# Optimization experiments

Hardware: AMD Instinct MI355X
Metric: run time of the kernel (lower is better)

Reference implementation:

```python
import jax, jax.numpy as jnp
import numpy as np

PS = 8  # patch_size
EPS = 1e-5


def _layernorm(t, w, b):
    m = jnp.mean(t, axis=-1, keepdims=True)
    v = jnp.mean((t - m) ** 2, axis=-1, keepdims=True)
    return (t - m) * jax.lax.rsqrt(v + EPS) * w + b


def _to3d(t):  # B(HW)C -> BCHW
    B, N, C = t.shape
    H = W = int(np.sqrt(N))
    return t.reshape(B, H, W, C).transpose(0, 3, 1, 2)


def _to2d(t):  # BCHW -> B(HW)C
    B, C, H, W = t.shape
    return t.reshape(B, C, H * W).swapaxes(-1, -2)


def _block(t, ps=PS):  # BCHW -> [B, M, ps*ps, C] (dilated-grid blocking, as in torch code)
    B, C, H, W = t.shape
    t = t.reshape(B, C, ps, H // ps, ps, W // ps)
    t = t.transpose(0, 3, 5, 2, 4, 1)
    return t.reshape(B, (H * W) // (ps * ps), ps * ps, C)


def _unblock(t):  # inverse of _block
    B, M, N, C = t.shape
    Hb = Wb = int(np.sqrt(M))
    ps = int(np.sqrt(N))
    t = t.reshape(B, Hb, Wb, ps, ps, C)
    t = t.transpose(0, 5, 3, 1, 4, 2)
    return t.reshape(B, C, Hb * ps, Wb * ps)


def setup_inputs() -> dict:
    key = jax.random.key(0)
    ks = jax.random.split(key, 8)
    B, N, D, H = 8, 4096, 256, 8
    s = 1.0 / np.sqrt(D)
    return {
        "x": jax.random.normal(ks[0], (B, N, D), jnp.float32),
        "ln1_w": jnp.ones((D,), jnp.float32),
        "ln1_b": jnp.zeros((D,), jnp.float32),
        "q": jax.random.normal(ks[1], (H, D, D), jnp.float32) * s,
        "k": jax.random.normal(ks[2], (D, D), jnp.float32) * s,
        "v": jax.random.normal(ks[3], (D, D), jnp.float32) * s,
        "o": jax.random.normal(ks[4], (H, D, D), jnp.float32) * s,
        "ln2_w": jnp.ones((D,), jnp.float32),
        "ln2_b": jnp.zeros((D,), jnp.float32),
        "w1": jax.random.normal(ks[5], (D, D), jnp.float32) * s,
        "b1": jnp.zeros((D,), jnp.float32),
        "w2": jax.random.normal(ks[6], (D, D), jnp.float32) * s,
        "b2": jnp.zeros((D,), jnp.float32),
    }


def reference(x, ln1_w, ln1_b, q, k, v, o, ln2_w, ln2_b, w1, b1, w2, b2):
    # blocked input: [B, M, P, D], M = HW/ps^2, P = ps^2
    a = _block(_to3d(_layernorm(x, ln1_w, ln1_b)))
    nh = q.shape[0]
    Q = jnp.einsum('bmnd,hdk->bhmnk', a, q)
    Q1, Q2 = Q[:, : nh // 2], Q[:, nh // 2 :]
    K = jnp.einsum('bmnd,dk->bmnk', a, k)
    V = jnp.einsum('bmnd,dv->bmnv', a, v)
    # axis 1: attend across blocks (m) at fixed within-block position (y=n)
    s1 = jax.nn.softmax(jnp.einsum('bhxyk,bzyk->bhyxz', Q1, K), axis=-1)
    O1 = jnp.einsum('bhyxz,bzyv->bhxyv', s1, V)
    # axis 2: attend within block (n) at fixed block (x=m)
    s2 = jax.nn.softmax(jnp.einsum('bhxyk,bxzk->bhxyz', Q2, K), axis=-1)
    O2 = jnp.einsum('bhxyz,bxzv->bhxyv', s2, V)
    O = jnp.concatenate([O1, O2], axis=1)  # [B, H, M, P, D]
    # faithful to torch: 'bhmnd,hdv->bmnd' sums over h and v
    Z = jnp.einsum('bhmnd,hdv->bmnd', O, o)
    x = x + _to2d(_unblock(Z))
    h = _layernorm(x, ln2_w, ln2_b)
    mlp = jax.nn.relu(h @ w1 + b1) @ w2 + b2
    return x + mlp
```

## Files before the change

### kernel.cpp

```cpp
#include <hip/hip_runtime.h>

#define Bc   8
#define Tc   4096
#define Dc   256
#define EPSc 1e-5f

typedef _Float16 half_t;
typedef __attribute__((ext_vector_type(4))) _Float16 half4_t;
typedef __attribute__((ext_vector_type(8))) _Float16 frag8;
typedef __attribute__((ext_vector_type(4))) float f32x4;

#define MFMA_F16(a, b, c) __builtin_amdgcn_mfma_f32_16x16x32_f16((a), (b), (c), 0, 0, 0)

__global__ __launch_bounds__(256) void osum_kernel(const float* __restrict__ o, float* __restrict__ os) {
  int h = blockIdx.x, d = threadIdx.x;
  const float* row = o + ((size_t)h * 256 + d) * 256;
  float s = 0.f;
  #pragma unroll 8
  for (int v = 0; v < 256; v += 4) {
    float4 r4 = *(const float4*)&row[v];
    s += r4.x + r4.y + r4.z + r4.w;
  }
  os[h * 256 + d] = s;
}

__global__ __launch_bounds__(256) void prepM_kernel(const float* __restrict__ q,
                                                    const float* __restrict__ k,
                                                    half_t* __restrict__ Mt) {
  __shared__ float shK[32 * 260];
  __shared__ float shQ[32 * 260];
  int tid = threadIdx.x;
  int h = blockIdx.x >> 6, et = (blockIdx.x >> 3) & 7, dt = blockIdx.x & 7;
  const float* kbase = k + (size_t)(et * 32) * 256;
  const float* qbase = q + ((size_t)h * 256 + dt * 32) * 256;
  #pragma unroll
  for (int r = 0; r < 8; r++) {
    int f = r * 256 + tid;
    int row = f >> 6, c4 = (f & 63) * 4;
    *(float4*)&shK[row * 260 + c4] = *(const float4*)&kbase[(size_t)row * 256 + c4];
    *(float4*)&shQ[row * 260 + c4] = *(const float4*)&qbase[(size_t)row * 256 + c4];
  }
  __syncthreads();
  int e = tid & 31, dg = tid >> 5;
  const float* kr = &shK[e * 260];
  const float* q0 = &shQ[(dg * 4 + 0) * 260];
  const float* q1 = &shQ[(dg * 4 + 1) * 260];
  const float* q2 = &shQ[(dg * 4 + 2) * 260];
  const float* q3 = &shQ[(dg * 4 + 3) * 260];
  float a0 = 0.f, a1 = 0.f, a2 = 0.f, a3 = 0.f;
  #pragma unroll 4
  for (int kk = 0; kk < 256; kk += 4) {
    float4 kv = *(const float4*)&kr[kk];
    float4 v0 = *(const float4*)&q0[kk];
    float4 v1 = *(const float4*)&q1[kk];
    float4 v2 = *(const float4*)&q2[kk];
    float4 v3 = *(const float4*)&q3[kk];
    a0 += v0.x * kv.x + v0.y * kv.y + v0.z * kv.z + v0.w * kv.w;
    a1 += v1.x * kv.x + v1.y * kv.y + v1.z * kv.z + v1.w * kv.w;
    a2 += v2.x * kv.x + v2.y * kv.y + v2.z * kv.z + v2.w * kv.w;
    a3 += v3.x * kv.x + v3.y * kv.y + v3.z * kv.z + v3.w * kv.w;
  }
  half4_t outv;
  outv[0] = (half_t)a0; outv[1] = (half_t)a1; outv[2] = (half_t)a2; outv[3] = (half_t)a3;
  *(half4_t*)&Mt[((size_t)h * 256 + et * 32 + e) * 256 + dt * 32 + dg * 4] = outv;
}

__global__ __launch_bounds__(256) void prepT_kernel(const float* __restrict__ v,
                                                    const float* __restrict__ w1,
                                                    const float* __restrict__ w2,
                                                    half_t* vt, half_t* w1t, half_t* w2t) {
  int which = blockIdx.x >> 8, n = blockIdx.x & 255, d = threadIdx.x;
  const float* src = which == 0 ? v : (which == 1 ? w1 : w2);
  half_t* dst = which == 0 ? vt : (which == 1 ? w1t : w2t);
  dst[(size_t)n * 256 + d] = (half_t)src[(size_t)d * 256 + n];
}

__global__ __launch_bounds__(256) void ln1_kernel(
    const float* __restrict__ x, const float* __restrict__ w,
    const float* __restrict__ bia, half_t* __restrict__ aH) {
  int row  = blockIdx.x * 4 + (threadIdx.x >> 6);
  int lane = threadIdx.x & 63;
  float4 v = *(const float4*)&x[(size_t)row * 256 + lane * 4];
  float s  = v.x + v.y + v.z + v.w;
  float sq = v.x * v.x + v.y * v.y + v.z * v.z + v.w * v.w;
  #pragma unroll
  for (int off = 1; off < 64; off <<= 1) { s += __shfl_xor(s, off); sq += __shfl_xor(sq, off); }
  float mean = s * (1.f / 256), var = sq * (1.f / 256) - mean * mean;
  float r = rsqrtf(var + EPSc);
  float4 wv = *(const float4*)&w[lane * 4];
  float4 bv = *(const float4*)&bia[lane * 4];
  half4_t y;
  y[0] = (half_t)((v.x - mean) * r * wv.x + bv.x);
  y[1] = (half_t)((v.y - mean) * r * wv.y + bv.y);
  y[2] = (half_t)((v.z - mean) * r * wv.z + bv.z);
  y[3] = (half_t)((v.w - mean) * r * wv.w + bv.w);
  int bb = row >> 12, p = row & 4095, hh = p >> 6, ww = p & 63;
  int m = (hh & 7) * 8 + (ww & 7), n = (hh >> 3) * 8 + (ww >> 3);
  *(half4_t*)&aH[((size_t)((bb * 64 + m) * 64 + n)) * 256 + lane * 4] = y;
}

__global__ __launch_bounds__(256) void wgemm_kernel(
    const half_t* __restrict__ A, const half_t* __restrict__ Bt,
    const float* __restrict__ bias, float* __restrict__ outf,
    half_t* __restrict__ outh, int epi, int ldn, int mtiles) {
  __shared__ half_t shA[128 * 72];
  __shared__ half_t shB[128 * 72];
  int tid = threadIdx.x, lane = tid & 63, wave = tid >> 6;
  int l16 = lane & 15, quad = lane >> 4;
  int mtile = blockIdx.x % mtiles, ntile = blockIdx.x / mtiles;
  int r0 = mtile * 128, n0 = ntile * 128;
  int wm = (wave >> 1) * 64, wn = (wave & 1) * 64;
  f32x4 acc[4][4];
  #pragma unroll
  for (int mt = 0; mt < 4; mt++)
    #pragma unroll
    for (int nt = 0; nt < 4; nt++) acc[mt][nt] = (f32x4){0.f, 0.f, 0.f, 0.f};
  for (int kb = 0; kb < 256; kb += 64) {
    if (kb) __syncthreads();
    #pragma unroll
    for (int rr = 0; rr < 4; rr++) {
      int idx = rr * 256 + tid;
      int row = idx >> 3, c8 = (idx & 7) * 8;
      *(frag8*)&shA[row * 72 + c8] = *(const frag8*)&A[(size_t)(r0 + row) * 256 + kb + c8];
      *(frag8*)&shB[row * 72 + c8] = *(const frag8*)&Bt[(size_t)(n0 + row) * 256 + kb + c8];
    }
    __syncthreads();
    #pragma unroll
    for (int kh = 0; kh < 2; kh++) {
      int ko = kh * 32 + quad * 8;
      frag8 af[4], bf[4];
      #pragma unroll
      for (int mt = 0; mt < 4; mt++) af[mt] = *(const frag8*)&shA[(wm + mt * 16 + l16) * 72 + ko];
      #pragma unroll
      for (int nt = 0; nt < 4; nt++) bf[nt] = *(const frag8*)&shB[(wn + nt * 16 + l16) * 72 + ko];
      #pragma unroll
      for (int mt = 0; mt < 4; mt++)
        #pragma unroll
        for (int nt = 0; nt < 4; nt++) acc[mt][nt] = MFMA_F16(af[mt], bf[nt], acc[mt][nt]);
    }
  }
  #pragma unroll
  for (int mt = 0; mt < 4; mt++)
    #pragma unroll
    for (int nt = 0; nt < 4; nt++)
      #pragma unroll
      for (int r = 0; r < 4; r++) {
        int row = r0 + wm + mt * 16 + quad * 4 + r;
        int col = n0 + wn + nt * 16 + l16;
        float vv = acc[mt][nt][r];
        if (epi) vv += bias[col];
        if (epi == 1) vv = fmaxf(vv, 0.f);
        size_t idx = (size_t)row * ldn + col;
        if (epi == 2) outf[idx] = vv + outf[idx];
        else          outh[idx] = (half_t)vv;
      }
}

__global__ __launch_bounds__(512, 2) void attn_kernel(
    const half_t* __restrict__ aH, const half_t* __restrict__ Mt,
    const half_t* __restrict__ vt, const float* __restrict__ osum,
    half_t* __restrict__ Z0, half_t* __restrict__ Z1) {
  __shared__ half_t shA[64 * 264];
  __shared__ half_t shU[64 * 264 + 64 * 72];
  half_t* shVT = shU;
  half_t* shW  = shU;
  half_t* shP  = shU + 64 * 264;
  int tid = threadIdx.x, lane = tid & 63, w = tid >> 6;
  int l16 = lane & 15, quad = lane >> 4;
  int g = blockIdx.x;
  int mode = g >> 9, gg = g & 511, b = gg >> 6, slice = gg & 63;
  int hbase = mode * 4;
  half_t* Z = mode ? Z1 : Z0;

  #pragma unroll
  for (int i = 0; i < 4; i++) {
    int slot = i * 512 + tid;
    int z = slot >> 5, c8 = (slot & 31) * 8;
    size_t rz = mode ? ((size_t)(b * 64 + slice) * 64 + z) : ((size_t)(b * 64 + z) * 64 + slice);
    *(frag8*)&shA[z * 264 + c8] = *(const frag8*)&aH[rz * 256 + c8];
  }

  frag8 vpre[2][8];
  #pragma unroll
  for (int ks = 0; ks < 8; ks++)
    #pragma unroll
    for (int dt = 0; dt < 2; dt++)
      vpre[dt][ks] = *(const frag8*)&vt[(size_t)(w * 32 + dt * 16 + l16) * 256 + ks * 32 + quad * 8];
  frag8 bfp[2][8];
  {
    const half_t* M0 = Mt + (size_t)hbase * 65536;
    #pragma unroll
    for (int et = 0; et < 2; et++)
      #pragma unroll
      for (int ks = 0; ks < 8; ks++)
        bfp[et][ks] = *(const frag8*)&M0[(size_t)(w * 32 + et * 16 + l16) * 256 + ks * 32 + quad * 8];
  }
  __builtin_amdgcn_sched_barrier(0);
  __syncthreads();

  {
    f32x4 vacc[2][4];
    #pragma unroll
    for (int dt = 0; dt < 2; dt++)
      #pragma unroll
      for (int zt = 0; zt < 4; zt++) vacc[dt][zt] = (f32x4){0.f, 0.f, 0.f, 0.f};
    #pragma unroll
    for (int ks = 0; ks < 8; ks++) {
      int k0 = ks * 32 + quad * 8;
      frag8 bfr[4];
      #pragma unroll
      for (int zt = 0; zt < 4; zt++)
        bfr[zt] = *(const frag8*)&shA[(zt * 16 + l16) * 264 + k0];
      #pragma unroll
      for (int dt = 0; dt < 2; dt++)
        #pragma unroll
        for (int zt = 0; zt < 4; zt++) vacc[dt][zt] = MFMA_F16(vpre[dt][ks], bfr[zt], vacc[dt][zt]);
    }
    #pragma unroll
    for (int dt = 0; dt < 2; dt++)
      #pragma unroll
      for (int zt = 0; zt < 4; zt++)
        #pragma unroll
        for (int r = 0; r < 4; r++)
          shVT[(w * 32 + dt * 16 + quad * 4 + r) * 72 + zt * 16 + l16] = (half_t)vacc[dt][zt][r];
  }
  __syncthreads();

  frag8 vtreg[2][2];
  #pragma unroll
  for (int dt = 0; dt < 2; dt++)
    #pragma unroll
    for (int ks = 0; ks < 2; ks++)
      vtreg[dt][ks] = *(const frag8*)&shVT[(w * 32 + dt * 16 + l16) * 72 + ks * 32 + quad * 8];

  float osv[4][2];
  #pragma unroll
  for (int hh = 0; hh < 4; hh++)
    #pragma unroll
    for (int dt = 0; dt < 2; dt++)
      osv[hh][dt] = osum[(hbase + hh) * 256 + w * 32 + dt * 16 + l16];

  f32x4 zacc[4][2];
  #pragma unroll
  for (int mf = 0; mf < 4; mf++)
    #pragma unroll
    for (int dt = 0; dt < 2; dt++) zacc[mf][dt] = (f32x4){0.f, 0.f, 0.f, 0.f};
  __syncthreads();

  #pragma unroll
  for (int hh = 0; hh < 4; hh++) {
    {
      f32x4 wacc[2][4];
      #pragma unroll
      for (int et = 0; et < 2; et++)
        #pragma unroll
        for (int mf = 0; mf < 4; mf++) wacc[et][mf] = (f32x4){0.f, 0.f, 0.f, 0.f};
      #pragma unroll
      for (int ks = 0; ks < 8; ks++) {
        int k0 = ks * 32 + quad * 8;
        frag8 af[4];
        #pragma unroll
        for (int mf = 0; mf < 4; mf++) af[mf] = *(const frag8*)&shA[(mf * 16 + l16) * 264 + k0];
        #pragma unroll
        for (int et = 0; et < 2; et++)
          #pragma unroll
          for (int mf = 0; mf < 4; mf++) wacc[et][mf] = MFMA_F16(af[mf], bfp[et][ks], wacc[et][mf]);
      }
      #pragma unroll
      for (int et = 0; et < 2; et++)
        #pragma unroll
        for (int mf = 0; mf < 4; mf++)
          #pragma unroll
          for (int r = 0; r < 4; r++)
            shW[(mf * 16 + quad * 4 + r) * 264 + w * 32 + et * 16 + l16] = (half_t)wacc[et][mf][r];
    }
    __syncthreads();
    if (hh < 3) {
      const half_t* Mn = Mt + (size_t)(hbase + hh + 1) * 65536;
      #pragma unroll
      for (int et = 0; et < 2; et++)
        #pragma unroll
        for (int ks = 0; ks < 8; ks++)
          bfp[et][ks] = *(const frag8*)&Mn[(size_t)(w * 32 + et * 16 + l16) * 256 + ks * 32 + quad * 8];
      __builtin_amdgcn_sched_barrier(0);
    }
    if (w < 4) {
      f32x4 sacc[4];
      #pragma unroll
      for (int zt = 0; zt < 4; zt++) sacc[zt] = (f32x4){0.f, 0.f, 0.f, 0.f};
      frag8 wf_all[8];
      #pragma unroll
      for (int ks = 0; ks < 8; ks++)
        wf_all[ks] = *(const frag8*)&shW[(w * 16 + l16) * 264 + ks * 32 + quad * 8];
      #pragma unroll
      for (int ks = 0; ks < 8; ks++) {
        int k0 = ks * 32 + quad * 8;
        #pragma unroll
        for (int zt = 0; zt < 4; zt++) {
          frag8 kf = *(const frag8*)&shA[(zt * 16 + l16) * 264 + k0];
          sacc[zt] = MFMA_F16(wf_all[ks], kf, sacc[zt]);
        }
      }
      #pragma unroll
      for (int r = 0; r < 4; r++) {
        float mx = fmaxf(fmaxf(sacc[0][r], sacc[1][r]), fmaxf(sacc[2][r], sacc[3][r]));
        #pragma unroll
        for (int off = 1; off < 16; off <<= 1) mx = fmaxf(mx, __shfl_xor(mx, off));
        float e0 = __expf(sacc[0][r] - mx), e1 = __expf(sacc[1][r] - mx);
        float e2 = __expf(sacc[2][r] - mx), e3 = __expf(sacc[3][r] - mx);
        float sum = e0 + e1 + e2 + e3;
        #pragma unroll
        for (int off = 1; off < 16; off <<= 1) sum += __shfl_xor(sum, off);
        float inv = 1.f / sum;
        int m = w * 16 + quad * 4 + r;
        shP[m * 72 + l16 +  0] = (half_t)(e0 * inv);
        shP[m * 72 + l16 + 16] = (half_t)(e1 * inv);
        shP[m * 72 + l16 + 32] = (half_t)(e2 * inv);
        shP[m * 72 + l16 + 48] = (half_t)(e3 * inv);
      }
    }
    __syncthreads();
    #pragma unroll
    for (int mf = 0; mf < 4; mf++) {
      frag8 pf0 = *(const frag8*)&shP[(mf * 16 + l16) * 72 +  0 + quad * 8];
      frag8 pf1 = *(const frag8*)&shP[(mf * 16 + l16) * 72 + 32 + quad * 8];
      #pragma unroll
      for (int dt = 0; dt < 2; dt++) {
        f32x4 oacc = (f32x4){0.f, 0.f, 0.f, 0.f};
        oacc = MFMA_F16(pf0, vtreg[dt][0], oacc);
        oacc = MFMA_F16(pf1, vtreg[dt][1], oacc);
        #pragma unroll
        for (int r = 0; r < 4; r++) zacc[mf][dt][r] += oacc[r] * osv[hh][dt];
      }
    }
  }

  #pragma unroll
  for (int mf = 0; mf < 4; mf++)
    #pragma unroll
    for (int dt = 0; dt < 2; dt++)
      #pragma unroll
      for (int r = 0; r < 4; r++)
        shA[(mf * 16 + quad * 4 + r) * 264 + w * 32 + dt * 16 + l16] = (half_t)zacc[mf][dt][r];
  __syncthreads();
  #pragma unroll
  for (int i = 0; i < 4; i++) {
    int slot = i * 512 + tid;
    int grow = slot >> 5, c8 = (slot & 31) * 8;
    size_t zrow = mode ? ((size_t)(b * 64 + slice) * 64 + grow) : ((size_t)(b * 64 + grow) * 64 + slice);
    *(frag8*)&Z[zrow * 256 + c8] = *(const frag8*)&shA[grow * 264 + c8];
  }
}

__global__ __launch_bounds__(256) void ln2_kernel(
    const float* __restrict__ x, const half_t* __restrict__ Z0, const half_t* __restrict__ Z1,
    const float* __restrict__ w, const float* __restrict__ bia,
    float* __restrict__ x2out, half_t* __restrict__ hH) {
  int row  = blockIdx.x * 4 + (threadIdx.x >> 6);
  int lane = threadIdx.x & 63;
  size_t base = (size_t)row * 256 + lane * 4;
  int bb = row >> 12, p = row & 4095, hh = p >> 6, ww = p & 63;
  int m = (hh & 7) * 8 + (ww & 7), n = (hh >> 3) * 8 + (ww >> 3);
  size_t zbase = ((size_t)((bb * 64 + m) * 64 + n)) * 256 + lane * 4;
  float4 xv = *(const float4*)&x[base];
  half4_t zv0 = *(const half4_t*)&Z0[zbase];
  half4_t zv1 = *(const half4_t*)&Z1[zbase];
  float4 v;
  v.x = xv.x + (float)zv0[0] + (float)zv1[0];
  v.y = xv.y + (float)zv0[1] + (float)zv1[1];
  v.z = xv.z + (float)zv0[2] + (float)zv1[2];
  v.w = xv.w + (float)zv0[3] + (float)zv1[3];
  float s  = v.x + v.y + v.z + v.w;
  float sq = v.x * v.x + v.y * v.y + v.z * v.z + v.w * v.w;
  #pragma unroll
  for (int off = 1; off < 64; off <<= 1) { s += __shfl_xor(s, off); sq += __shfl_xor(sq, off); }
  float mean = s * (1.f / 256), var = sq * (1.f / 256) - mean * mean;
  float r = rsqrtf(var + EPSc);
  float4 wv = *(const float4*)&w[lane * 4];
  float4 bv = *(const float4*)&bia[lane * 4];
  *(float4*)&x2out[base] = v;
  half4_t y;
  y[0] = (half_t)((v.x - mean) * r * wv.x + bv.x);
  y[1] = (half_t)((v.y - mean) * r * wv.y + bv.y);
  y[2] = (half_t)((v.z - mean) * r * wv.z + bv.z);
  y[3] = (half_t)((v.w - mean) * r * wv.w + bv.w);
  *(half4_t*)&hH[base] = y;
}

extern "C" void kernel_launch(void* const* d_in, const int* in_sizes, int n_in,
                              void* d_out, int out_size, void* d_ws, size_t ws_size,
                              hipStream_t stream) {
  (void)in_sizes; (void)n_in; (void)out_size; (void)ws_size;
  const float* x    = (const float*)d_in[0];
  const float* ln1w = (const float*)d_in[1];
  const float* ln1b = (const float*)d_in[2];
  const float* q    = (const float*)d_in[3];
  const float* k    = (const float*)d_in[4];
  const float* v    = (const float*)d_in[5];
  const float* o    = (const float*)d_in[6];
  const float* ln2w = (const float*)d_in[7];
  const float* ln2b = (const float*)d_in[8];
  const float* w1   = (const float*)d_in[9];
  const float* b1   = (const float*)d_in[10];
  const float* w2   = (const float*)d_in[11];
  const float* b2   = (const float*)d_in[12];
  float* out = (float*)d_out;

  const size_t ROWS = (size_t)Bc * Tc;
  const size_t ELTS = ROWS * Dc;
  const size_t MB16 = ELTS * sizeof(half_t);
  char* ws = (char*)d_ws;
  float*  osumB = (float*)ws;
  half_t* Mt    = (half_t*)(ws + (64 << 10));
  half_t* vt    = (half_t*)(ws + (64 << 10) + (1 << 20));
  half_t* w1t   = (half_t*)(ws + (64 << 10) + (1 << 20) + (128 << 10));
  half_t* w2t   = (half_t*)(ws + (64 << 10) + (1 << 20) + (256 << 10));
  half_t* aH    = (half_t*)(ws + (2 << 20));
  half_t* Zb0   = (half_t*)(ws + (2 << 20) + MB16);
  half_t* Zb1   = (half_t*)(ws + (2 << 20) + 2 * MB16);
  half_t* hH    = aH;
  half_t* tH    = Zb1;

  osum_kernel <<<8,   256, 0, stream>>>(o, osumB);
  prepM_kernel<<<512, 256, 0, stream>>>(q, k, Mt);
  prepT_kernel<<<768, 256, 0, stream>>>(v, w1, w2, vt, w1t, w2t);
  ln1_kernel  <<<ROWS / 4, 256, 0, stream>>>(x, ln1w, ln1b, aH);
  attn_kernel <<<1024, 512, 0, stream>>>(aH, Mt, vt, osumB, Zb0, Zb1);
  ln2_kernel  <<<ROWS / 4, 256, 0, stream>>>(x, Zb0, Zb1, ln2w, ln2b, out, hH);
  wgemm_kernel<<<512, 256, 0, stream>>>(hH, w1t, b1, nullptr, tH, 1, 256, 256);
  wgemm_kernel<<<512, 256, 0, stream>>>(tH, w2t, b2, out, nullptr, 2, 256, 256);
}
```

Baseline: 315.5 us.

## Halve attention block to 4 waves, each wave covering 64 output columns

The attention kernel now runs with 256 threads (4 waves) instead of 512. Each wave covers twice the columns in the V projection, the W=aM projection (split into two halves with reloads of the M fragments) and the output accumulation. All four waves now do the score/softmax stage, where previously half the waves sat idle there. The aim is more work per wave, fewer idle waves and cheaper barriers, at the cost of more registers per thread (zacc doubles) and more serialized MFMA work per wave, which may lower occupancy and latency hiding.

```diff
diff --git a/kernel.cpp b/kernel.cpp
--- a/kernel.cpp
+++ b/kernel.cpp
@@ -156,7 +156,7 @@
       }
 }
 
-__global__ __launch_bounds__(512, 2) void attn_kernel(
+__global__ __launch_bounds__(256, 2) void attn_kernel(
     const half_t* __restrict__ aH, const half_t* __restrict__ Mt,
     const half_t* __restrict__ vt, const float* __restrict__ osum,
     half_t* __restrict__ Z0, half_t* __restrict__ Z1) {
@@ -173,88 +173,89 @@
   half_t* Z = mode ? Z1 : Z0;
 
   #pragma unroll
-  for (int i = 0; i < 4; i++) {
-    int slot = i * 512 + tid;
+  for (int i = 0; i < 8; i++) {
+    int slot = i * 256 + tid;
     int z = slot >> 5, c8 = (slot & 31) * 8;
     size_t rz = mode ? ((size_t)(b * 64 + slice) * 64 + z) : ((size_t)(b * 64 + z) * 64 + slice);
     *(frag8*)&shA[z * 264 + c8] = *(const frag8*)&aH[rz * 256 + c8];
   }
-
-  frag8 vpre[2][8];
-  #pragma unroll
-  for (int ks = 0; ks < 8; ks++)
-    #pragma unroll
-    for (int dt = 0; dt < 2; dt++)
-      vpre[dt][ks] = *(const frag8*)&vt[(size_t)(w * 32 + dt * 16 + l16) * 256 + ks * 32 + quad * 8];
+  __syncthreads();
+
+  #pragma unroll
+  for (int dth = 0; dth < 2; dth++) {
+    frag8 vpre[2][8];
+    #pragma unroll
+    for (int dt2 = 0; dt2 < 2; dt2++)
+      #pragma unroll
+      for (int ks = 0; ks < 8; ks++)
+        vpre[dt2][ks] = *(const frag8*)&vt[(size_t)(w * 64 + dth * 32 + dt2 * 16 + l16) * 256 + ks * 32 + quad * 8];
+    f32x4 vacc[2][4];
+    #pragma unroll
+    for (int dt2 = 0; dt2 < 2; dt2++)
+      #pragma unroll
+      for (int zt = 0; zt < 4; zt++) vacc[dt2][zt] = (f32x4){0.f, 0.f, 0.f, 0.f};
+    #pragma unroll
+    for (int ks = 0; ks < 8; ks++) {
+      int k0 = ks * 32 + quad * 8;
+      frag8 bfr[4];
+      #pragma unroll
+      for (int zt = 0; zt < 4; zt++)
+        bfr[zt] = *(const frag8*)&shA[(zt * 16 + l16) * 264 + k0];
+      #pragma unroll
+      for (int dt2 = 0; dt2 < 2; dt2++)
+        #pragma unroll
+        for (int zt = 0; zt < 4; zt++) vacc[dt2][zt] = MFMA_F16(vpre[dt2][ks], bfr[zt], vacc[dt2][zt]);
+    }
+    #pragma unroll
+    for (int dt2 = 0; dt2 < 2; dt2++)
+      #pragma unroll
+      for (int zt = 0; zt < 4; zt++)
+        #pragma unroll
+        for (int r = 0; r < 4; r++)
+          shVT[(w * 64 + dth * 32 + dt2 * 16 + quad * 4 + r) * 72 + zt * 16 + l16] = (half_t)vacc[dt2][zt][r];
+  }
+  __syncthreads();
+
+  frag8 vtreg[4][2];
+  #pragma unroll
+  for (int dt = 0; dt < 4; dt++)
+    #pragma unroll
+    for (int ks = 0; ks < 2; ks++)
+      vtreg[dt][ks] = *(const frag8*)&shVT[(w * 64 + dt * 16 + l16) * 72 + ks * 32 + quad * 8];
+
+  float osv[4][4];
+  #pragma unroll
+  for (int hh = 0; hh < 4; hh++)
+    #pragma unroll
+    for (int dt = 0; dt < 4; dt++)
+      osv[hh][dt] = osum[(hbase + hh) * 256 + w * 64 + dt * 16 + l16];
+
+  f32x4 zacc[4][4];
+  #pragma unroll
+  for (int mf = 0; mf < 4; mf++)
+    #pragma unroll
+    for (int dt = 0; dt < 4; dt++) zacc[mf][dt] = (f32x4){0.f, 0.f, 0.f, 0.f};
+  __syncthreads();
+
   frag8 bfp[2][8];
   {
     const half_t* M0 = Mt + (size_t)hbase * 65536;
     #pragma unroll
-    for (int et = 0; et < 2; et++)
+    for (int et2 = 0; et2 < 2; et2++)
       #pragma unroll
       for (int ks = 0; ks < 8; ks++)
-        bfp[et][ks] = *(const frag8*)&M0[(size_t)(w * 32 + et * 16 + l16) * 256 + ks * 32 + quad * 8];
-  }
-  __builtin_amdgcn_sched_barrier(0);
-  __syncthreads();
-
-  {
-    f32x4 vacc[2][4];
-    #pragma unroll
-    for (int dt = 0; dt < 2; dt++)
-      #pragma unroll
-      for (int zt = 0; zt < 4; zt++) vacc[dt][zt] = (f32x4){0.f, 0.f, 0.f, 0.f};
-    #pragma unroll
-    for (int ks = 0; ks < 8; ks++) {
-      int k0 = ks * 32 + quad * 8;
-      frag8 bfr[4];
-      #pragma unroll
-      for (int zt = 0; zt < 4; zt++)
-        bfr[zt] = *(const frag8*)&shA[(zt * 16 + l16) * 264 + k0];
-      #pragma unroll
-      for (int dt = 0; dt < 2; dt++)
-        #pragma unroll
-        for (int zt = 0; zt < 4; zt++) vacc[dt][zt] = MFMA_F16(vpre[dt][ks], bfr[zt], vacc[dt][zt]);
-    }
-    #pragma unroll
-    for (int dt = 0; dt < 2; dt++)
-      #pragma unroll
-      for (int zt = 0; zt < 4; zt++)
-        #pragma unroll
-        for (int r = 0; r < 4; r++)
-          shVT[(w * 32 + dt * 16 + quad * 4 + r) * 72 + zt * 16 + l16] = (half_t)vacc[dt][zt][r];
-  }
-  __syncthreads();
-
-  frag8 vtreg[2][2];
-  #pragma unroll
-  for (int dt = 0; dt < 2; dt++)
-    #pragma unroll
-    for (int ks = 0; ks < 2; ks++)
-      vtreg[dt][ks] = *(const frag8*)&shVT[(w * 32 + dt * 16 + l16) * 72 + ks * 32 + quad * 8];
-
-  float osv[4][2];
-  #pragma unroll
-  for (int hh = 0; hh < 4; hh++)
-    #pragma unroll
-    for (int dt = 0; dt < 2; dt++)
-      osv[hh][dt] = osum[(hbase + hh) * 256 + w * 32 + dt * 16 + l16];
-
-  f32x4 zacc[4][2];
-  #pragma unroll
-  for (int mf = 0; mf < 4; mf++)
-    #pragma unroll
-    for (int dt = 0; dt < 2; dt++) zacc[mf][dt] = (f32x4){0.f, 0.f, 0.f, 0.f};
-  __syncthreads();
+        bfp[et2][ks] = *(const frag8*)&M0[(size_t)(w * 64 + et2 * 16 + l16) * 256 + ks * 32 + quad * 8];
+  }
 
   #pragma unroll
   for (int hh = 0; hh < 4; hh++) {
+    const half_t* Mth = Mt + (size_t)(hbase + hh) * 65536;
     {
       f32x4 wacc[2][4];
       #pragma unroll
-      for (int et = 0; et < 2; et++)
-        #pragma unroll
-        for (int mf = 0; mf < 4; mf++) wacc[et][mf] = (f32x4){0.f, 0.f, 0.f, 0.f};
+      for (int et2 = 0; et2 < 2; et2++)
+        #pragma unroll
+        for (int mf = 0; mf < 4; mf++) wacc[et2][mf] = (f32x4){0.f, 0.f, 0.f, 0.f};
       #pragma unroll
       for (int ks = 0; ks < 8; ks++) {
         int k0 = ks * 32 + quad * 8;
@@ -262,29 +263,60 @@
         #pragma unroll
         for (int mf = 0; mf < 4; mf++) af[mf] = *(const frag8*)&shA[(mf * 16 + l16) * 264 + k0];
         #pragma unroll
-        for (int et = 0; et < 2; et++)
+        for (int et2 = 0; et2 < 2; et2++)
           #pragma unroll
-          for (int mf = 0; mf < 4; mf++) wacc[et][mf] = MFMA_F16(af[mf], bfp[et][ks], wacc[et][mf]);
-      }
-      #pragma unroll
-      for (int et = 0; et < 2; et++)
+          for (int mf = 0; mf < 4; mf++) wacc[et2][mf] = MFMA_F16(af[mf], bfp[et2][ks], wacc[et2][mf]);
+      }
+      #pragma unroll
+      for (int et2 = 0; et2 < 2; et2++)
+        #pragma unroll
+        for (int ks = 0; ks < 8; ks++)
+          bfp[et2][ks] = *(const frag8*)&Mth[(size_t)(w * 64 + 32 + et2 * 16 + l16) * 256 + ks * 32 + quad * 8];
+      __builtin_amdgcn_sched_barrier(0);
+      #pragma unroll
+      for (int et2 = 0; et2 < 2; et2++)
         #pragma unroll
         for (int mf = 0; mf < 4; mf++)
           #pragma unroll
           for (int r = 0; r < 4; r++)
-            shW[(mf * 16 + quad * 4 + r) * 264 + w * 32 + et * 16 + l16] = (half_t)wacc[et][mf][r];
+            shW[(mf * 16 + quad * 4 + r) * 264 + w * 64 + et2 * 16 + l16] = (half_t)wacc[et2][mf][r];
+    }
+    {
+      f32x4 wacc[2][4];
+      #pragma unroll
+      for (int et2 = 0; et2 < 2; et2++)
+        #pragma unroll
+        for (int mf = 0; mf < 4; mf++) wacc[et2][mf] = (f32x4){0.f, 0.f, 0.f, 0.f};
+      #pragma unroll
+      for (int ks = 0; ks < 8; ks++) {
+        int k0 = ks * 32 + quad * 8;
+        frag8 af[4];
+        #pragma unroll
+        for (int mf = 0; mf < 4; mf++) af[mf] = *(const frag8*)&shA[(mf * 16 + l16) * 264 + k0];
+        #pragma unroll
+        for (int et2 = 0; et2 < 2; et2++)
+          #pragma unroll
+          for (int mf = 0; mf < 4; mf++) wacc[et2][mf] = MFMA_F16(af[mf], bfp[et2][ks], wacc[et2][mf]);
+      }
+      #pragma unroll
+      for (int et2 = 0; et2 < 2; et2++)
+        #pragma unroll
+        for (int mf = 0; mf < 4; mf++)
+          #pragma unroll
+          for (int r = 0; r < 4; r++)
+            shW[(mf * 16 + quad * 4 + r) * 264 + w * 64 + 32 + et2 * 16 + l16] = (half_t)wacc[et2][mf][r];
     }
     __syncthreads();
     if (hh < 3) {
       const half_t* Mn = Mt + (size_t)(hbase + hh + 1) * 65536;
       #pragma unroll
-      for (int et = 0; et < 2; et++)
+      for (int et2 = 0; et2 < 2; et2++)
         #pragma unroll
         for (int ks = 0; ks < 8; ks++)
-          bfp[et][ks] = *(const frag8*)&Mn[(size_t)(w * 32 + et * 16 + l16) * 256 + ks * 32 + quad * 8];
+          bfp[et2][ks] = *(const frag8*)&Mn[(size_t)(w * 64 + et2 * 16 + l16) * 256 + ks * 32 + quad * 8];
       __builtin_amdgcn_sched_barrier(0);
     }
-    if (w < 4) {
+    {
       f32x4 sacc[4];
       #pragma unroll
       for (int zt = 0; zt < 4; zt++) sacc[zt] = (f32x4){0.f, 0.f, 0.f, 0.f};
@@ -325,7 +357,7 @@
       frag8 pf0 = *(const frag8*)&shP[(mf * 16 + l16) * 72 +  0 + quad * 8];
       frag8 pf1 = *(const frag8*)&shP[(mf * 16 + l16) * 72 + 32 + quad * 8];
       #pragma unroll
-      for (int dt = 0; dt < 2; dt++) {
+      for (int dt = 0; dt < 4; dt++) {
         f32x4 oacc = (f32x4){0.f, 0.f, 0.f, 0.f};
         oacc = MFMA_F16(pf0, vtreg[dt][0], oacc);
         oacc = MFMA_F16(pf1, vtreg[dt][1], oacc);
@@ -338,14 +370,14 @@
   #pragma unroll
   for (int mf = 0; mf < 4; mf++)
     #pragma unroll
-    for (int dt = 0; dt < 2; dt++)
+    for (int dt = 0; dt < 4; dt++)
       #pragma unroll
       for (int r = 0; r < 4; r++)
-        shA[(mf * 16 + quad * 4 + r) * 264 + w * 32 + dt * 16 + l16] = (half_t)zacc[mf][dt][r];
+        shA[(mf * 16 + quad * 4 + r) * 264 + w * 64 + dt * 16 + l16] = (half_t)zacc[mf][dt][r];
   __syncthreads();
   #pragma unroll
-  for (int i = 0; i < 4; i++) {
-    int slot = i * 512 + tid;
+  for (int i = 0; i < 8; i++) {
+    int slot = i * 256 + tid;
     int grow = slot >> 5, c8 = (slot & 31) * 8;
     size_t zrow = mode ? ((size_t)(b * 64 + slice) * 64 + grow) : ((size_t)(b * 64 + grow) * 64 + slice);
     *(frag8*)&Z[zrow * 256 + c8] = *(const frag8*)&shA[grow * 264 + c8];
@@ -425,7 +457,7 @@
   prepM_kernel<<<512, 256, 0, stream>>>(q, k, Mt);
   prepT_kernel<<<768, 256, 0, stream>>>(v, w1, w2, vt, w1t, w2t);
   ln1_kernel  <<<ROWS / 4, 256, 0, stream>>>(x, ln1w, ln1b, aH);
-  attn_kernel <<<1024, 512, 0, stream>>>(aH, Mt, vt, osumB, Zb0, Zb1);
+  attn_kernel <<<1024, 256, 0, stream>>>(aH, Mt, vt, osumB, Zb0, Zb1);
   ln2_kernel  <<<ROWS / 4, 256, 0, stream>>>(x, Zb0, Zb1, ln2w, ln2b, out, hH);
   wgemm_kernel<<<512, 256, 0, stream>>>(hH, w1t, b1, nullptr, tH, 1, 256, 256);
   wgemm_kernel<<<512, 256, 0, stream>>>(tH, w2t, b2, out, nullptr, 2, 256, 256);
```

Measured after the change: 357.4 us. 1.13x slower.
